# Kernel optimization log

Hardware: AMD Instinct MI355X
Metric: run time of the kernel (lower is better)

The kernel has to match this reference:

```python
import jax, jax.numpy as jnp
import numpy as np
from jax import lax

H_SP, W_SP = 32, 8   # idx == 0
NUM_HEADS = 2
DIM = 64
SCALE = (DIM // NUM_HEADS) ** -0.5


def conv1x1(x, w, b):
    # x: [B,C,H,W], w: [O,C,1,1], b: [O]
    return jnp.einsum('bchw,oc->bohw', x, w[:, :, 0, 0]) + b[None, :, None, None]


def dwconv5(x, w, b):
    # depthwise 5x5, pad 2. w: [C,1,5,5]
    y = lax.conv_general_dilated(
        x, w, window_strides=(1, 1), padding=[(2, 2), (2, 2)],
        dimension_numbers=('NCHW', 'OIHW', 'NCHW'),
        feature_group_count=x.shape[1])
    return y + b[None, :, None, None]


def im2cswin(x):
    # [B,C,H,W] -> [B*nH*nW, heads, H_SP*W_SP, C//heads]
    B, C, H, W = x.shape
    x = x.reshape(B, C, H // H_SP, H_SP, W // W_SP, W_SP)
    x = x.transpose(0, 2, 4, 3, 5, 1).reshape(-1, H_SP * W_SP, NUM_HEADS, C // NUM_HEADS)
    return x.transpose(0, 2, 1, 3)


def windows2img(xw, H, W):
    # [B', H_SP*W_SP, C] -> [B, C, H, W]
    B = xw.shape[0] // ((H // H_SP) * (W // W_SP))
    x = xw.reshape(B, H // H_SP, W // W_SP, H_SP, W_SP, -1)
    return x.transpose(0, 5, 1, 3, 2, 4).reshape(B, -1, H, W)


def setup_inputs() -> dict:
    key = jax.random.key(0)
    ks = jax.random.split(key, 8)
    B, C, H, W = 4, DIM, 256, 256
    s = 0.02
    return {
        'x': jax.random.normal(ks[0], (B, C, H, W), dtype=jnp.float32),
        'qk_w': jax.random.normal(ks[1], (2 * C, C, 1, 1), dtype=jnp.float32) * s,
        'qk_b': jnp.zeros((2 * C,), jnp.float32),
        'q5_w': jax.random.normal(ks[2], (C, 1, 5, 5), dtype=jnp.float32) * s,
        'q5_b': jnp.zeros((C,), jnp.float32),
        'k5_w': jax.random.normal(ks[3], (C, 1, 5, 5), dtype=jnp.float32) * s,
        'k5_b': jnp.zeros((C,), jnp.float32),
        'v_w': jax.random.normal(ks[4], (C, C, 1, 1), dtype=jnp.float32) * s,
        'v_b': jnp.zeros((C,), jnp.float32),
        'lepe_w': jax.random.normal(ks[5], (C, 1, 5, 5), dtype=jnp.float32) * s,
        'lepe_b': jnp.zeros((C,), jnp.float32),
    }


def reference(x, qk_w, qk_b, q5_w, q5_b, k5_w, k5_b, v_w, v_b, lepe_w, lepe_b):
    B, C, H, W = x.shape
    pad_r = (W_SP - W % W_SP) % W_SP
    pad_b = (H_SP - H % H_SP) % H_SP
    xp = jnp.pad(x, ((0, 0), (0, 0), (0, pad_b), (0, pad_r)))
    Hp, Wp = xp.shape[2], xp.shape[3]
    # shift_size == 0 -> no roll
    qk = conv1x1(xp, qk_w, qk_b)
    q, k = jnp.split(qk, 2, axis=1)
    v = conv1x1(xp, v_w, v_b)
    lepe = dwconv5(v, lepe_w, lepe_b)
    qw = im2cswin(dwconv5(q, q5_w, q5_b) + lepe)   # [nw, h, N, d]
    kw = im2cswin(dwconv5(k, k5_w, k5_b) + lepe)
    vw = im2cswin(v)
    attn = jnp.einsum('whnd,whmd->whnm', qw * SCALE, kw)
    attn = jax.nn.softmax(attn, axis=-1)
    out = jnp.einsum('whnm,whmd->whnd', attn, vw)
    out = out.transpose(0, 2, 1, 3).reshape(-1, H_SP * W_SP, C)
    out = windows2img(out, Hp, Wp) + lepe
    if pad_r or pad_b:
        out = out[:, :, :H, :W]
    return out
```

## Files before the change

### kernel.cpp

```cpp
#include <hip/hip_runtime.h>


typedef unsigned short u16;
typedef short s16x8 __attribute__((ext_vector_type(8)));
typedef float f32x4 __attribute__((ext_vector_type(4)));

#define MFMA16(a, b, c) __builtin_amdgcn_mfma_f32_16x16x32_bf16((a), (b), (c), 0, 0, 0)

#define SCALE_F 0.17677669529663687f

__device__ __forceinline__ u16 f2bf(float f) {
  unsigned u = __float_as_uint(f);
  return (u16)((u + 0x7FFFu + ((u >> 16) & 1u)) >> 16);
}
__device__ __forceinline__ float bf2f(u16 h) {
  return __uint_as_float(((unsigned)h) << 16);
}

__global__ __launch_bounds__(256, 4) void k1_conv1x1(
    const float* __restrict__ x, const float* __restrict__ qk_w,
    const float* __restrict__ qk_b, const float* __restrict__ v_w,
    const float* __restrict__ v_b, u16* __restrict__ qkv) {
  __shared__ u16 Wl[12288];
  __shared__ float Bl[192];
  int t = threadIdx.x;
  for (int i = t; i < 12288; i += 256) {
    int oc = i >> 6, ic = i & 63;
    float wv_ = (oc < 128) ? qk_w[i] : v_w[i - 8192];
    Wl[(oc << 6) | (ic ^ ((oc & 7) << 3))] = f2bf(wv_);
  }
  if (t < 192) Bl[t] = (t < 128) ? qk_b[t] : v_b[t - 128];
  __syncthreads();

  int lane = t & 63, wv = t >> 6;
  int col = lane & 15, g = lane >> 4;
  int p0 = blockIdx.x * 64 + wv * 16;
  int b = p0 >> 16, pix0 = p0 & 65535;

  const float* xb = x + (size_t)b * 4194304 + pix0 + col;
  s16x8 bfrag[2];
#pragma unroll
  for (int kk = 0; kk < 2; ++kk) {
#pragma unroll
    for (int j = 0; j < 8; ++j) {
      int ic = kk * 32 + g * 8 + j;
      bfrag[kk][j] = (short)f2bf(xb[(size_t)ic << 16]);
    }
  }

  f32x4 acc[12];
#pragma unroll
  for (int mt = 0; mt < 12; ++mt) acc[mt] = 0.f;
#pragma unroll
  for (int mt = 0; mt < 12; ++mt) {
    int oc = mt * 16 + col;
    int swz = (oc & 7) << 3;
#pragma unroll
    for (int kk = 0; kk < 2; ++kk) {
      s16x8 af = *(const s16x8*)&Wl[(oc << 6) | ((kk * 32 + g * 8) ^ swz)];
      acc[mt] = MFMA16(af, bfrag[kk], acc[mt]);
    }
  }

  u16* ob = qkv + (size_t)b * 12582912 + pix0 + col;
#pragma unroll
  for (int mt = 0; mt < 12; ++mt) {
#pragma unroll
    for (int r = 0; r < 4; ++r) {
      int oc = mt * 16 + g * 4 + r;
      ob[(size_t)oc << 16] = f2bf(acc[mt][r] + Bl[oc]);
    }
  }
}


__device__ __forceinline__ int qt_off(int tok, int d) {
  return (tok << 5) + (d ^ (((tok >> 2) & 3) << 3));
}
__device__ __forceinline__ int vt_off(int d, int tok) {
  int swz = (((d & 7) ^ ((tok >> 6) & 3)) << 3);
  return (d << 8) + ((tok & ~7) ^ swz) + (tok & 7);
}

__global__ __launch_bounds__(512, 4) void k23_fused(
    const u16* __restrict__ qkv, const float* __restrict__ q5_w,
    const float* __restrict__ q5_b, const float* __restrict__ k5_w,
    const float* __restrict__ k5_b, const float* __restrict__ lepe_w,
    const float* __restrict__ lepe_b, float* __restrict__ out) {
  __shared__ u16 SM[38912];
  u16* QT = SM;
  u16* KT = SM + 8192;
  u16* VT = SM + 16384;
  u16* LT = SM + 24576;
  u16* HS = SM + 32768;
  u16* WLb = SM + 36224;
  float* BLf = (float*)(SM + 38720);

  int raw = blockIdx.x;
  int bid = (raw & 7) * 256 + (raw >> 3);
  int head = bid & 1, wj = (bid >> 1) & 31, wi = (bid >> 6) & 7, b = bid >> 9;
  int h0 = wi * 32, w0 = wj * 8;

  int t = threadIdx.x;
  int wv = t >> 6, lane = t & 63;
  int dl = lane & 7, tq = lane >> 3;
  const size_t bbase = (size_t)b * 12582912;

  for (int i = t; i < 2400; i += 512) {
    int ts = i / 800, rem = i - ts * 800, ch = rem / 25, j = rem - ch * 25;
    const float* srcw = (ts == 0 ? lepe_w : ts == 1 ? q5_w : k5_w);
    WLb[ts * 832 + ch * 26 + j] = f2bf(srcw[(head * 32 + ch) * 25 + j]);
  }
  if (t < 96) {
    int ts = t >> 5, ch = t & 31;
    BLf[t] = (ts == 0 ? lepe_b : ts == 1 ? q5_b : k5_b)[head * 32 + ch];
  }

  unsigned fixOff[4], okm[4];
  int ldsOff[4];
  bool live[4];
#pragma unroll
  for (int it = 0; it < 4; ++it) {
    int ip = t + it * 512;
    live[it] = ip < 1728;
    int ipc = live[it] ? ip : 0;
    int ch = ipc / 216, rem = ipc - ch * 216;
    int hr = rem / 6, hc = rem - hr * 6;
    int gh = h0 - 2 + hr, gw = w0 - 2 + hc * 2;
    bool ok = live[it] & ((unsigned)gh < 256u) & ((unsigned)gw <= 254u);
    int hcl = gh < 0 ? 0 : (gh > 255 ? 255 : gh);
    int wcl = gw < 0 ? 0 : (gw > 254 ? 254 : gw);
    fixOff[it] = ((unsigned)ch << 16) + hcl * 256 + wcl;
    okm[it] = ok ? 0xffffffffu : 0u;
    ldsOff[it] = (ch * 36 + hr) * 12 + hc * 2;
  }

  unsigned cr[4];
  auto stage_ld = [&](int p) {
    int cg = p / 3, ts = p - cg * 3;
    int planeBase = (ts == 0 ? 128 : ts == 1 ? 0 : 64) + head * 32 + cg * 8;
    const u16* src = qkv + bbase + ((size_t)planeBase << 16);
#pragma unroll
    for (int it = 0; it < 4; ++it)
      if (live[it]) {
        unsigned v = *(const unsigned*)&src[fixOff[it]];
        cr[it] = v & okm[it];
      }
  };
  auto stage_st = [&]() {
#pragma unroll
    for (int it = 0; it < 4; ++it)
      if (live[it]) *(unsigned*)&HS[ldsOff[it]] = cr[it];
  };

  stage_ld(0);
  stage_st();
  __syncthreads();

  int row = wv * 4 + (tq >> 1), c0 = (tq & 1) * 4;
  int tok0 = wv * 32 + tq * 4;
  float lepA[4];

#pragma unroll 1
  for (int p = 0; p < 12; ++p) {
    if (p < 11) stage_ld(p + 1);
    int cg = p / 3, ts = p - cg * 3;
    int d = cg * 8 + dl;

    float wr[25];
    {
      const u16* wb = &WLb[ts * 832 + d * 26];
#pragma unroll
      for (int k2 = 0; k2 < 12; ++k2) {
        unsigned u = *(const unsigned*)&wb[k2 * 2];
        wr[2 * k2] = __uint_as_float(u << 16);
        wr[2 * k2 + 1] = __uint_as_float(u & 0xffff0000u);
      }
      wr[24] = bf2f(wb[24]);
    }
    float bias = BLf[ts * 32 + d];

    const u16* hb = &HS[(dl * 36 + row) * 12 + c0];
    float acc[4] = {bias, bias, bias, bias};
    float ctr[4];
#pragma unroll
    for (int i = 0; i < 5; ++i) {
      uint2 A = *(const uint2*)&hb[i * 12];
      uint2 Bv = *(const uint2*)&hb[i * 12 + 4];
      float px[8];
      px[0] = __uint_as_float(A.x << 16);
      px[1] = __uint_as_float(A.x & 0xffff0000u);
      px[2] = __uint_as_float(A.y << 16);
      px[3] = __uint_as_float(A.y & 0xffff0000u);
      px[4] = __uint_as_float(Bv.x << 16);
      px[5] = __uint_as_float(Bv.x & 0xffff0000u);
      px[6] = __uint_as_float(Bv.y << 16);
      px[7] = __uint_as_float(Bv.y & 0xffff0000u);
      if (ts == 0 && i == 2) {
#pragma unroll
        for (int j = 0; j < 4; ++j) ctr[j] = px[j + 2];
      }
#pragma unroll
      for (int jj = 0; jj < 5; ++jj) {
        float w5 = wr[i * 5 + jj];
#pragma unroll
        for (int j = 0; j < 4; ++j) acc[j] = fmaf(px[j + jj], w5, acc[j]);
      }
    }

    if (ts == 0) {
      uint2 ov, ol;
      ov.x = (unsigned)f2bf(ctr[0]) | ((unsigned)f2bf(ctr[1]) << 16);
      ov.y = (unsigned)f2bf(ctr[2]) | ((unsigned)f2bf(ctr[3]) << 16);
      ol.x = (unsigned)f2bf(acc[0]) | ((unsigned)f2bf(acc[1]) << 16);
      ol.y = (unsigned)f2bf(acc[2]) | ((unsigned)f2bf(acc[3]) << 16);
      *(uint2*)&VT[vt_off(d, tok0)] = ov;
      *(uint2*)&LT[vt_off(d, tok0)] = ol;
#pragma unroll
      for (int j = 0; j < 4; ++j) lepA[j] = acc[j];
    } else {
      u16* tile = (ts == 1) ? QT : KT;
#pragma unroll
      for (int j = 0; j < 4; ++j) {
        float o = acc[j] + lepA[j];
        if (ts == 1) o *= SCALE_F;
        tile[qt_off(tok0 + j, d)] = f2bf(o);
      }
    }
    __syncthreads();
    if (p < 11) {
      stage_st();
      __syncthreads();
    }
  }

  int col = lane & 15, g = lane >> 4;
  int rbase = wv * 32;

  s16x8 qa[2];
  float lepr[2][8];
#pragma unroll
  for (int mt = 0; mt < 2; ++mt) {
    int tok = rbase + mt * 16 + col;
    qa[mt] = *(const s16x8*)&QT[qt_off(tok, g * 8)];
#pragma unroll
    for (int dt = 0; dt < 2; ++dt)
#pragma unroll
      for (int r = 0; r < 4; ++r) {
        int d = dt * 16 + g * 4 + r;
        lepr[mt][dt * 4 + r] = bf2f(LT[vt_off(d, tok)]);
      }
  }
  __syncthreads();

  u16* Pw = (wv < 4) ? (SM + wv * 2048) : (SM + 24576 + (wv - 4) * 2048);
  float* ob = out + (((size_t)(b * 64 + head * 32)) << 16) + h0 * 256 + w0;

#pragma unroll 1
  for (int mt = 0; mt < 2; ++mt) {
    int row0 = rbase + mt * 16;
    f32x4 zero = 0.f;
    f32x4 sacc[16];
#pragma unroll
    for (int nt = 0; nt < 16; ++nt) {
      int tj = nt * 16 + col;
      s16x8 kb = *(const s16x8*)&KT[qt_off(tj, g * 8)];
      sacc[nt] = MFMA16(qa[mt], kb, zero);
    }
    float mx[4], sm[4];
#pragma unroll
    for (int r = 0; r < 4; ++r) {
      float m = sacc[0][r];
#pragma unroll
      for (int nt = 1; nt < 16; ++nt) m = fmaxf(m, sacc[nt][r]);
#pragma unroll
      for (int s = 1; s < 16; s <<= 1) m = fmaxf(m, __shfl_xor(m, s));
      mx[r] = m;
    }
#pragma unroll
    for (int r = 0; r < 4; ++r) {
      float s0 = 0.f;
#pragma unroll
      for (int nt = 0; nt < 16; ++nt) {
        float p = exp2f((sacc[nt][r] - mx[r]) * 1.4426950408889634f);
        sacc[nt][r] = p;
        s0 += p;
      }
#pragma unroll
      for (int s = 1; s < 16; s <<= 1) s0 += __shfl_xor(s0, s);
      sm[r] = 1.f / s0;
    }

    f32x4 oacc[2];
    oacc[0] = 0.f;
    oacc[1] = 0.f;
#pragma unroll
    for (int chunk = 0; chunk < 2; ++chunk) {
#pragma unroll
      for (int r = 0; r < 4; ++r) {
        int irow = g * 4 + r;
        int swz = (irow & 7) << 3;
#pragma unroll
        for (int ntl = 0; ntl < 8; ++ntl)
          Pw[irow * 128 + ((ntl * 16 + col) ^ swz)] =
              f2bf(sacc[chunk * 8 + ntl][r] * sm[r]);
      }
#pragma unroll
      for (int ks = 0; ks < 4; ++ks) {
        int kc = ks * 32 + g * 8;
        s16x8 pb = *(const s16x8*)&Pw[col * 128 + (kc ^ ((col & 7) << 3))];
#pragma unroll
        for (int dt = 0; dt < 2; ++dt) {
          int dls = dt * 16 + col;
          s16x8 va = *(const s16x8*)&VT[vt_off(dls, chunk * 128 + kc)];
          oacc[dt] = MFMA16(va, pb, oacc[dt]);
        }
      }
    }
    int tok = row0 + col;
#pragma unroll
    for (int dt = 0; dt < 2; ++dt) {
#pragma unroll
      for (int r = 0; r < 4; ++r) {
        int d = dt * 16 + g * 4 + r;
        float val = oacc[dt][r] + lepr[mt][dt * 4 + r];
        ob[((size_t)d << 16) + (tok >> 3) * 256 + (tok & 7)] = val;
      }
    }
  }
}

extern "C" void kernel_launch(void* const* d_in, const int* in_sizes, int n_in,
                              void* d_out, int out_size, void* d_ws,
                              size_t ws_size, hipStream_t stream) {
  const float* x = (const float*)d_in[0];
  const float* qk_w = (const float*)d_in[1];
  const float* qk_b = (const float*)d_in[2];
  const float* q5_w = (const float*)d_in[3];
  const float* q5_b = (const float*)d_in[4];
  const float* k5_w = (const float*)d_in[5];
  const float* k5_b = (const float*)d_in[6];
  const float* v_w = (const float*)d_in[7];
  const float* v_b = (const float*)d_in[8];
  const float* lepe_w = (const float*)d_in[9];
  const float* lepe_b = (const float*)d_in[10];
  float* out = (float*)d_out;

  if (ws_size < 100663296ull) return;
  u16* qkv = (u16*)d_ws;

  hipLaunchKernelGGL(k1_conv1x1, dim3(4096), dim3(256), 0, stream, x, qk_w,
                     qk_b, v_w, v_b, qkv);
  hipLaunchKernelGGL(k23_fused, dim3(2048), dim3(512), 0, stream, qkv, q5_w,
                     q5_b, k5_w, k5_b, lepe_w, lepe_b, out);
}
```

Baseline: 228.3 us.

## Defer softmax normalization, pack P as bf16 pairs, permute V token order

Moves the softmax 1/sum scaling from each probability element to the final output by fetching the row sum through a shuffle and applying a reciprocal in an FMA. P is packed as two bf16 values per 32-bit LDS store, which requires the V tile to be stored in a permuted token order so the PV MFMA k-dimension still lines up. It also swaps in hardware exp2 and rcp builtins, folds the max subtraction into an FMA, and packs the Q/K/V bf16 conversions. The aim is fewer ALU ops and fewer LDS stores in the attention inner loop. The cost is scalar scattered stores for V and an extra cross-lane shuffle, plus reduced precision from the approximate exp2 and rcp.

Measured after the change: 215.4 us. 1.06x faster.

```diff
diff --git a/kernel.cpp b/kernel.cpp
--- a/kernel.cpp
+++ b/kernel.cpp
@@ -8,6 +8,19 @@
 #define MFMA16(a, b, c) __builtin_amdgcn_mfma_f32_16x16x32_bf16((a), (b), (c), 0, 0, 0)
 
 #define SCALE_F 0.17677669529663687f
+#define LOG2E_F 1.4426950408889634f
+
+#if __has_builtin(__builtin_amdgcn_exp2f)
+#define EXP2F(x) __builtin_amdgcn_exp2f(x)
+#else
+#define EXP2F(x) exp2f(x)
+#endif
+
+#if __has_builtin(__builtin_amdgcn_rcpf)
+#define RCPF(x) __builtin_amdgcn_rcpf(x)
+#else
+#define RCPF(x) (1.f / (x))
+#endif
 
 __device__ __forceinline__ u16 f2bf(float f) {
   unsigned u = __float_as_uint(f);
@@ -15,6 +28,12 @@
 }
 __device__ __forceinline__ float bf2f(u16 h) {
   return __uint_as_float(((unsigned)h) << 16);
+}
+__device__ __forceinline__ unsigned pk_rne(float lo, float hi) {
+  unsigned ul = __float_as_uint(lo), uh = __float_as_uint(hi);
+  ul += 0x7FFFu + ((ul >> 16) & 1u);
+  uh += 0x7FFFu + ((uh >> 16) & 1u);
+  return (ul >> 16) | (uh & 0xFFFF0000u);
 }
 
 __global__ __launch_bounds__(256, 4) void k1_conv1x1(
@@ -209,23 +228,34 @@
     }
 
     if (ts == 0) {
-      uint2 ov, ol;
-      ov.x = (unsigned)f2bf(ctr[0]) | ((unsigned)f2bf(ctr[1]) << 16);
-      ov.y = (unsigned)f2bf(ctr[2]) | ((unsigned)f2bf(ctr[3]) << 16);
-      ol.x = (unsigned)f2bf(acc[0]) | ((unsigned)f2bf(acc[1]) << 16);
-      ol.y = (unsigned)f2bf(acc[2]) | ((unsigned)f2bf(acc[3]) << 16);
-      *(uint2*)&VT[vt_off(d, tok0)] = ov;
+      uint2 ol;
+      ol.x = pk_rne(acc[0], acc[1]);
+      ol.y = pk_rne(acc[2], acc[3]);
       *(uint2*)&LT[vt_off(d, tok0)] = ol;
+      unsigned pv01 = pk_rne(ctr[0], ctr[1]), pv23 = pk_rne(ctr[2], ctr[3]);
+      int aa = tok0 >> 5, h2 = (tok0 >> 4) & 1, cc = tok0 & 15;
+      int sb = aa * 32 + cc * 2 + h2;
+      VT[vt_off(d, sb)] = (u16)pv01;
+      VT[vt_off(d, sb + 2)] = (u16)(pv01 >> 16);
+      VT[vt_off(d, sb + 4)] = (u16)pv23;
+      VT[vt_off(d, sb + 6)] = (u16)(pv23 >> 16);
 #pragma unroll
       for (int j = 0; j < 4; ++j) lepA[j] = acc[j];
     } else {
       u16* tile = (ts == 1) ? QT : KT;
-#pragma unroll
-      for (int j = 0; j < 4; ++j) {
-        float o = acc[j] + lepA[j];
-        if (ts == 1) o *= SCALE_F;
-        tile[qt_off(tok0 + j, d)] = f2bf(o);
-      }
+      float o0 = acc[0] + lepA[0], o1 = acc[1] + lepA[1];
+      float o2 = acc[2] + lepA[2], o3 = acc[3] + lepA[3];
+      if (ts == 1) {
+        o0 *= SCALE_F;
+        o1 *= SCALE_F;
+        o2 *= SCALE_F;
+        o3 *= SCALE_F;
+      }
+      unsigned q01 = pk_rne(o0, o1), q23 = pk_rne(o2, o3);
+      tile[qt_off(tok0, d)] = (u16)q01;
+      tile[qt_off(tok0 + 1, d)] = (u16)(q01 >> 16);
+      tile[qt_off(tok0 + 2, d)] = (u16)q23;
+      tile[qt_off(tok0 + 3, d)] = (u16)(q23 >> 16);
     }
     __syncthreads();
     if (p < 11) {
@@ -267,52 +297,68 @@
       s16x8 kb = *(const s16x8*)&KT[qt_off(tj, g * 8)];
       sacc[nt] = MFMA16(qa[mt], kb, zero);
     }
-    float mx[4], sm[4];
+    float mx[4];
 #pragma unroll
     for (int r = 0; r < 4; ++r) {
       float m = sacc[0][r];
 #pragma unroll
-      for (int nt = 1; nt < 16; ++nt) m = fmaxf(m, sacc[nt][r]);
+      for (int nt = 1; nt < 15; nt += 2)
+        m = fmaxf(m, fmaxf(sacc[nt][r], sacc[nt + 1][r]));
+      m = fmaxf(m, sacc[15][r]);
 #pragma unroll
       for (int s = 1; s < 16; s <<= 1) m = fmaxf(m, __shfl_xor(m, s));
       mx[r] = m;
     }
+    float ssum[4];
 #pragma unroll
     for (int r = 0; r < 4; ++r) {
+      float cm = -mx[r] * LOG2E_F;
       float s0 = 0.f;
 #pragma unroll
       for (int nt = 0; nt < 16; ++nt) {
-        float p = exp2f((sacc[nt][r] - mx[r]) * 1.4426950408889634f);
-        sacc[nt][r] = p;
-        s0 += p;
+        float pv = EXP2F(fmaf(sacc[nt][r], LOG2E_F, cm));
+        sacc[nt][r] = pv;
+        s0 += pv;
       }
 #pragma unroll
       for (int s = 1; s < 16; s <<= 1) s0 += __shfl_xor(s0, s);
-      sm[r] = 1.f / s0;
-    }
+      ssum[r] = s0;
+    }
+    int srcl = (col >> 2) << 4;
+    float t0 = __shfl(ssum[0], srcl);
+    float t1 = __shfl(ssum[1], srcl);
+    float t2 = __shfl(ssum[2], srcl);
+    float t3 = __shfl(ssum[3], srcl);
+    float sA = (col & 1) ? t1 : t0;
+    float sB = (col & 1) ? t3 : t2;
+    float inv = RCPF((col & 2) ? sB : sA);
 
     f32x4 oacc[2];
     oacc[0] = 0.f;
     oacc[1] = 0.f;
+    unsigned* PwU = (unsigned*)Pw;
 #pragma unroll
     for (int chunk = 0; chunk < 2; ++chunk) {
 #pragma unroll
       for (int r = 0; r < 4; ++r) {
         int irow = g * 4 + r;
-        int swz = (irow & 7) << 3;
-#pragma unroll
-        for (int ntl = 0; ntl < 8; ++ntl)
-          Pw[irow * 128 + ((ntl * 16 + col) ^ swz)] =
-              f2bf(sacc[chunk * 8 + ntl][r] * sm[r]);
+        int wb = irow * 64;
+        int sw = (irow & 7) << 2;
+#pragma unroll
+        for (int al = 0; al < 4; ++al) {
+          int nt = chunk * 8 + al * 2;
+          PwU[wb + ((al * 16 + col) ^ sw)] =
+              pk_rne(sacc[nt][r], sacc[nt + 1][r]);
+        }
       }
 #pragma unroll
       for (int ks = 0; ks < 4; ++ks) {
-        int kc = ks * 32 + g * 8;
-        s16x8 pb = *(const s16x8*)&Pw[col * 128 + (kc ^ ((col & 7) << 3))];
+        int kcp = (ks * 16 + g * 4) ^ ((col & 7) << 2);
+        s16x8 pb = *(const s16x8*)&PwU[col * 64 + kcp];
+        int sig = chunk * 128 + ks * 32 + g * 8;
 #pragma unroll
         for (int dt = 0; dt < 2; ++dt) {
-          int dls = dt * 16 + col;
-          s16x8 va = *(const s16x8*)&VT[vt_off(dls, chunk * 128 + kc)];
+          s16x8 va = *(const s16x8*)&VT[vt_off(dt * 16 + col, sig)];
           oacc[dt] = MFMA16(va, pb, oacc[dt]);
         }
       }
@@ -323,7 +369,7 @@
 #pragma unroll
       for (int r = 0; r < 4; ++r) {
         int d = dt * 16 + g * 4 + r;
-        float val = oacc[dt][r] + lepr[mt][dt * 4 + r];
+        float val = fmaf(oacc[dt][r], inv, lepr[mt][dt * 4 + r]);
         ob[((size_t)d << 16) + (tok >> 3) * 256 + (tok & 7)] = val;
       }
     }
```
